# Kernel tuning notes

Measured on AMD Instinct MI355X. Metric: run time of the kernel, lower is better.

The kernel has to match this reference:

```python
import jax, jax.numpy as jnp
import numpy as np
from jax import lax

B, N, W = 32, 512, 256
C = 16            # branch channels; D = 4*C = 64
Z = 8             # SAE latent
E = 8             # sensor embedding dim
HD = 16           # GAT head dim = max(8, 32//2)
GOUT = 32         # GAT out dim
TOPK = 20
RHO, EPS = 0.05, 1e-6
KS = [2, 3, 5, 7]


def _glorot(key, shape):
    fan_in, fan_out = shape[0], shape[-1]
    lim = jnp.sqrt(6.0 / (fan_in + fan_out))
    return jax.random.uniform(key, shape, jnp.float32, -lim, lim)


def setup_inputs() -> dict:
    key = jax.random.key(0)
    ks = jax.random.split(key, 32)
    inp = {"x": jax.random.normal(ks[0], (B, N, W), jnp.float32)}
    # MSTCN conv weights: torch Conv1d weight [C, 1, k], bias [C]
    for i, k in enumerate(KS):
        inp[f"conv_w{k}"] = jax.random.normal(ks[1 + i], (C, 1, k), jnp.float32) * (1.0 / np.sqrt(k))
        inp[f"conv_b{k}"] = jnp.zeros((C,), jnp.float32)
    inp["enc_w"] = _glorot(ks[6], (4 * C, Z));  inp["enc_b"] = jnp.zeros((Z,), jnp.float32)
    inp["dec_w"] = _glorot(ks[7], (Z, W));      inp["dec_b"] = jnp.zeros((W,), jnp.float32)
    inp["sensor_emb"] = _glorot(ks[8], (N, E))
    gin = Z + E
    inp["gat0_w"] = _glorot(ks[9], (gin, HD))
    inp["gat0_asrc"] = _glorot(ks[10], (1, HD))[0]
    inp["gat0_adst"] = _glorot(ks[11], (1, HD))[0]
    inp["gat1_w"] = _glorot(ks[12], (gin, HD))
    inp["gat1_asrc"] = _glorot(ks[13], (1, HD))[0]
    inp["gat1_adst"] = _glorot(ks[14], (1, HD))[0]
    inp["proj_w"] = _glorot(ks[15], (2 * HD, GOUT)); inp["proj_b"] = jnp.zeros((GOUT,), jnp.float32)
    inp["head_w"] = _glorot(ks[16], (GOUT, 1));      inp["head_b"] = jnp.zeros((1,), jnp.float32)
    return inp


def _mstcn(x, convs):
    # x: [B,N,W] -> node_feat [B,N,4C]
    b, n, w = x.shape
    xr = x.reshape(b * n, 1, w)
    feats = []
    for (cw, cb), k in zip(convs, KS):
        pl = (k - 1) // 2
        pr = (k - 1) - pl
        y = lax.conv_general_dilated(xr, cw, (1,), [(pl, pr)],
                                     dimension_numbers=("NCH", "OIH", "NCH"))
        y = y + cb[None, :, None]                 # [B*N, C, W]
        feats.append(y.mean(-1).reshape(b, n, C)) # time mean -> [B,N,C]
    return jnp.concatenate(feats, -1)


def _graph_learning(sensor_emb):
    # returns A [N,N]
    nrm = jnp.sqrt(jnp.sum(sensor_emb * sensor_emb, -1, keepdims=True))
    emb = sensor_emb / jnp.maximum(nrm, 1e-12)
    sim = (emb @ emb.T) / jnp.sqrt(jnp.float32(E))
    n = sim.shape[0]
    sim_ns = sim.at[jnp.diag_indices(n)].set(-jnp.inf)
    idx = lax.top_k(sim_ns, TOPK)[1]                       # [N, topk]
    mask = jnp.zeros_like(sim).at[jnp.arange(n)[:, None], idx].set(1.0)
    return jax.nn.relu(sim) * mask + jnp.eye(n, dtype=sim.dtype)


def _gat_head(x, a, w, a_src, a_dst):
    # x [B,N,F], a [N,N] -> [B,N,HD]; eval mode (dropout off)
    h = x @ w                                   # [B,N,HD]
    e_src = h @ a_src                           # [B,N]
    e_dst = h @ a_dst                           # [B,N]
    e = jax.nn.leaky_relu(e_src[:, :, None] + e_dst[:, None, :], 0.2)  # [B,N,N]
    e = jnp.where((a > 0)[None], e, -jnp.inf)
    alpha = jax.nn.softmax(e, axis=-1)
    return alpha @ h


def reference(x, conv_w2, conv_b2, conv_w3, conv_b3, conv_w5, conv_b5,
              conv_w7, conv_b7, enc_w, enc_b, dec_w, dec_b, sensor_emb,
              gat0_w, gat0_asrc, gat0_adst, gat1_w, gat1_asrc, gat1_adst,
              proj_w, proj_b, head_w, head_b):
    convs = [(conv_w2, conv_b2), (conv_w3, conv_b3), (conv_w5, conv_b5), (conv_w7, conv_b7)]
    node_feat = _mstcn(x, convs)                           # [B,N,64]
    # Sparse autoencoder
    z = node_feat @ enc_w + enc_b                          # [B,N,Z]
    recon = z @ dec_w + dec_b                              # [B,N,W]
    act = jax.nn.sigmoid(z)
    rho_hat = jnp.clip(act.mean((0, 1)), EPS, 1.0 - EPS)
    kl = jnp.sum(RHO * jnp.log(RHO / rho_hat) + (1.0 - RHO) * jnp.log((1.0 - RHO) / (1.0 - rho_hat)))
    sparsity_dev = jnp.mean(jnp.abs(act - RHO), -1)        # [B,N]
    # Graph learning + GAT
    a = _graph_learning(sensor_emb)                        # [N,N]
    e_b = jnp.broadcast_to(sensor_emb[None], (x.shape[0], N, E))
    gat_in = jnp.concatenate([z, e_b], -1)                 # [B,N,Z+E]
    h0 = _gat_head(gat_in, a, gat0_w, gat0_asrc, gat0_adst)
    h1 = _gat_head(gat_in, a, gat1_w, gat1_asrc, gat1_adst)
    h = jnp.concatenate([h0, h1], -1)
    fused = jax.nn.elu(h @ proj_w + proj_b)                # [B,N,GOUT]
    predicted = (fused @ head_w + head_b)[..., 0]          # [B,N]
    return predicted, recon, kl, sparsity_dev
```

## Files before the change

### kernel.cpp

```cpp
#include <hip/hip_runtime.h>
#include <math.h>

#define B_   32
#define N_   512
#define W_   256
#define BN_  (B_*N_)
#define NBLK_A 2048
#define RHOG   2048

__device__ __forceinline__ float wave_reduce_sum64(float v) {
#pragma unroll
    for (int m = 32; m >= 1; m >>= 1) v += __shfl_xor(v, m);
    return v;
}

__global__ __launch_bounds__(256) void kPre(
    const float* __restrict__ se,
    const float* __restrict__ w2, const float* __restrict__ b2,
    const float* __restrict__ w3, const float* __restrict__ b3,
    const float* __restrict__ w5, const float* __restrict__ b5,
    const float* __restrict__ w7, const float* __restrict__ b7,
    const float* __restrict__ enc_w, const float* __restrict__ enc_b,
    const float* __restrict__ g0w, const float* __restrict__ g0s, const float* __restrict__ g0d,
    const float* __restrict__ g1w, const float* __restrict__ g1s, const float* __restrict__ g1d,
    float* __restrict__ en_g, float* __restrict__ ws_gam,
    float* __restrict__ ws_gsz, float* __restrict__ ws_gA)
{
    const int tid = threadIdx.x;

    if (blockIdx.x == 0) {
#pragma unroll
        for (int p = 0; p < 2; ++p) {
            const int rr = tid + p * 256;
            const float4 a = reinterpret_cast<const float4*>(se)[rr * 2];
            const float4 b = reinterpret_cast<const float4*>(se)[rr * 2 + 1];
            const float ss = a.x*a.x + a.y*a.y + a.z*a.z + a.w*a.w
                           + b.x*b.x + b.y*b.y + b.z*b.z + b.w*b.w;
            const float inv = 1.0f / fmaxf(sqrtf(ss), 1e-12f);
            float4 oa = a, ob = b;
            oa.x*=inv; oa.y*=inv; oa.z*=inv; oa.w*=inv;
            ob.x*=inv; ob.y*=inv; ob.z*=inv; ob.w*=inv;
            reinterpret_cast<float4*>(en_g)[rr * 2]     = oa;
            reinterpret_cast<float4*>(en_g)[rr * 2 + 1] = ob;
        }
        return;
    }

    __shared__ float L[1432];
    const int oW2=0, oW3=32, oW5=80, oW7=160;
    const int oB2=272, oB3=288, oB5=304, oB7=320;
    const int oEW=336, oEB=848, oG0=856, oG1=1112, oAV=1368;
#define CPY(off, src, n) for (int t = tid; t < (n); t += 256) L[(off)+t] = (src)[t];
    CPY(oW2, w2, 32)  CPY(oW3, w3, 48)  CPY(oW5, w5, 80)  CPY(oW7, w7, 112)
    CPY(oB2, b2, 16)  CPY(oB3, b3, 16)  CPY(oB5, b5, 16)  CPY(oB7, b7, 16)
    CPY(oEW, enc_w, 512)  CPY(oEB, enc_b, 8)
    CPY(oG0, g0w, 256)    CPY(oG1, g1w, 256)
    CPY(oAV, g0s, 16) CPY(oAV+16, g0d, 16) CPY(oAV+32, g1s, 16) CPY(oAV+48, g1d, 16)
#undef CPY
    __syncthreads();

    if (tid < 64) {
        const int zi = tid & 7, t = tid >> 3;
        float acc = (t == 7) ? L[oEB + zi] : 0.f;
#define GAM_KI(BASE_C, OFFW, OFFB, KK)                                          \
        {                                                                       \
            const int k = KK; const int pl = (k - 1) >> 1;                      \
            _Pragma("unroll")                                                   \
            for (int ch = 0; ch < 16; ++ch) {                                   \
                float a;                                                        \
                if (t == 7) a = L[OFFB + ch];                                   \
                else if (t == 0) {                                              \
                    a = 0.f;                                                    \
                    _Pragma("unroll")                                           \
                    for (int j = 0; j < k; ++j) a += L[OFFW + ch*k + j];        \
                    a *= (1.f/(float)W_);                                       \
                } else if (t <= 3) {                                            \
                    const int j = pl + t;                                       \
                    a = (j < k) ? -L[OFFW + ch*k + j]*(1.f/(float)W_) : 0.f;    \
                } else {                                                        \
                    const int j = pl - (t - 3);                                 \
                    a = (j >= 0) ? -L[OFFW + ch*k + j]*(1.f/(float)W_) : 0.f;   \
                }                                                               \
                acc += a * L[oEW + (BASE_C + ch)*8 + zi];                       \
            }                                                                   \
        }
        GAM_KI(0,  oW2, oB2, 2)
        GAM_KI(16, oW3, oB3, 3)
        GAM_KI(32, oW5, oB5, 5)
        GAM_KI(48, oW7, oB7, 7)
#undef GAM_KI
        ws_gam[zi*8+t] = acc;
    } else if (tid < 96) {
        const int q = (tid-64) >> 3, f = (tid-64) & 7;
        const int gw = (q >> 1) ? oG1 : oG0;
        const int av = oAV + q*16;
        float v = 0.f;
#pragma unroll
        for (int d = 0; d < 16; ++d) v += L[gw + f*16+d] * L[av + d];
        ws_gsz[q*8+f] = v;
    } else if (tid < 128) {
        const int q = (tid-96) >> 3, f = (tid-96) & 7;
        const int gw = (q >> 1) ? oG1 : oG0;
        const int av = oAV + q*16;
        float v = 0.f;
#pragma unroll
        for (int d = 0; d < 16; ++d) v += L[gw + (8+f)*16+d] * L[av + d];
        ws_gA[q*8+f] = v;
    }
}

__global__ __launch_bounds__(256) void kTop(const float* __restrict__ en_g,
                                            int* __restrict__ adj)
{
    const int wave = threadIdx.x >> 6;
    const int lane = threadIdx.x & 63;
    const int i = (blockIdx.x << 2) + wave;

    const float4 ei0 = reinterpret_cast<const float4*>(en_g)[i * 2];
    const float4 ei1 = reinterpret_cast<const float4*>(en_g)[i * 2 + 1];

    float v[8];
#pragma unroll
    for (int q = 0; q < 8; ++q) {
        const int j = (q << 6) + lane;
        const float4 a = reinterpret_cast<const float4*>(en_g)[j * 2];
        const float4 b = reinterpret_cast<const float4*>(en_g)[j * 2 + 1];
        const float d = ei0.x*a.x + ei0.y*a.y + ei0.z*a.z + ei0.w*a.w
                      + ei1.x*b.x + ei1.y*b.y + ei1.z*b.z + ei1.w*b.w;
        v[q] = (j == i) ? -3.4e38f : d * 0.35355339059327373f;
    }

    int cnt = 1;
    if (lane == 0) adj[i * 24 + 1] = i;
    for (int it = 0; it < 20; ++it) {
        float bv = v[0]; int bq = 0;
#pragma unroll
        for (int q = 1; q < 8; ++q) if (v[q] > bv) { bv = v[q]; bq = q; }
        int bj = (bq << 6) + lane;
#pragma unroll
        for (int m = 32; m >= 1; m >>= 1) {
            const float ov = __shfl_xor(bv, m);
            const int   oj = __shfl_xor(bj, m);
            if (ov > bv || (ov == bv && oj < bj)) { bv = ov; bj = oj; }
        }
        if (bv <= 0.f) break;
        if (lane == 0) adj[i * 24 + 1 + cnt] = bj;
        cnt++;
        const int wq = bj >> 6, wl = bj & 63;
#pragma unroll
        for (int q = 0; q < 8; ++q) if (q == wq && lane == wl) v[q] = -3.4e38f;
    }
    if (lane == 0) adj[i * 24] = cnt;
}

__global__ __launch_bounds__(256) void kA(
    const float* __restrict__ x,
    const float* __restrict__ dec_w, const float* __restrict__ dec_b,
    const float* __restrict__ g0w, const float* __restrict__ g1w,
    const float* __restrict__ se,
    const float* __restrict__ ws_gam, const float* __restrict__ ws_gsz,
    const float* __restrict__ ws_gA,
    float* __restrict__ out_recon, float* __restrict__ out_sdev,
    float* __restrict__ ws_h, float* __restrict__ ws_e, float* __restrict__ ws_rho)
{
    __shared__ float lds_rho[4][8];
    const int wave = threadIdx.x >> 6;
    const int lane = threadIdx.x & 63;
    const int r0 = (blockIdx.x << 3) + (wave << 1);
    const int n0 = r0 & (N_ - 1), n1 = (r0 + 1) & (N_ - 1);

    const float4 xv0 = reinterpret_cast<const float4*>(x)[(size_t)r0 * 64 + lane];
    const float4 xv1 = reinterpret_cast<const float4*>(x)[(size_t)(r0+1) * 64 + lane];
    const float4 ph0 = reinterpret_cast<const float4*>(x)[(size_t)r0 * 64];
    const float4 pt0 = reinterpret_cast<const float4*>(x)[(size_t)r0 * 64 + 63];
    const float4 ph1 = reinterpret_cast<const float4*>(x)[(size_t)(r0+1) * 64];
    const float4 pt1 = reinterpret_cast<const float4*>(x)[(size_t)(r0+1) * 64 + 63];

    float S0 = xv0.x + xv0.y + xv0.z + xv0.w;
    float S1 = xv1.x + xv1.y + xv1.z + xv1.w;
#pragma unroll
    for (int m = 32; m >= 1; m >>= 1) { S0 += __shfl_xor(S0, m); S1 += __shfl_xor(S1, m); }

    const float P10 = ph0.x, P20 = P10 + ph0.y, P30 = P20 + ph0.z;
    const float Q10 = pt0.w, Q20 = Q10 + pt0.z, Q30 = Q20 + pt0.y;
    const float P11 = ph1.x, P21 = P11 + ph1.y, P31 = P21 + ph1.z;
    const float Q11 = pt1.w, Q21 = Q11 + pt1.z, Q31 = Q21 + pt1.y;

    float z0[8], z1[8];
#pragma unroll
    for (int zi = 0; zi < 8; ++zi) {
        const float4 g0 = reinterpret_cast<const float4*>(ws_gam)[zi * 2];
        const float4 g1 = reinterpret_cast<const float4*>(ws_gam)[zi * 2 + 1];
        z0[zi] = g1.w + g0.x*S0 + g0.y*P10 + g0.z*P20 + g0.w*P30
                       + g1.x*Q10 + g1.y*Q20 + g1.z*Q30;
        z1[zi] = g1.w + g0.x*S1 + g0.y*P11 + g0.z*P21 + g0.w*P31
                       + g1.x*Q11 + g1.y*Q21 + g1.z*Q31;
    }

    {
        const float4 db = reinterpret_cast<const float4*>(dec_b)[lane];
        float4 rec0 = db, rec1 = db;
#pragma unroll
        for (int zi = 0; zi < 8; ++zi) {
            const float4 dw = reinterpret_cast<const float4*>(dec_w)[zi * 64 + lane];
            rec0.x += z0[zi]*dw.x; rec0.y += z0[zi]*dw.y; rec0.z += z0[zi]*dw.z; rec0.w += z0[zi]*dw.w;
            rec1.x += z1[zi]*dw.x; rec1.y += z1[zi]*dw.y; rec1.z += z1[zi]*dw.z; rec1.w += z1[zi]*dw.w;
        }
        reinterpret_cast<float4*>(out_recon)[(size_t)r0 * 64 + lane] = rec0;
        reinterpret_cast<float4*>(out_recon)[(size_t)(r0+1) * 64 + lane] = rec1;
    }

    if (lane < 16) {
        const int zi = lane & 7;
        const int rr = lane >> 3;
        float zl = 0.f;
#pragma unroll
        for (int p = 0; p < 8; ++p)
            zl = (zi == p) ? (rr ? z1[p] : z0[p]) : zl;
        const float a = 1.0f / (1.0f + __expf(-zl));
        float sd = fabsf(a - 0.05f);
        sd += __shfl_xor(sd, 1); sd += __shfl_xor(sd, 2); sd += __shfl_xor(sd, 4);
        if (zi == 0) out_sdev[r0 + rr] = sd * 0.125f;
        const float rho = a + __shfl_xor(a, 8);
        if (lane < 8) lds_rho[wave][lane] = rho;
    }

    if (lane < 32) {
        const float* gw = (lane >> 4) ? g1w : g0w;
        const int dd = lane & 15;
        float gwz[16];
#pragma unroll
        for (int f = 0; f < 16; ++f) gwz[f] = gw[f * 16 + dd];
        float h0 = 0.f, h1 = 0.f;
#pragma unroll
        for (int f = 0; f < 8; ++f) { h0 += z0[f] * gwz[f]; h1 += z1[f] * gwz[f]; }
#pragma unroll
        for (int f = 0; f < 8; ++f) {
            h0 += se[n0 * 8 + f] * gwz[8 + f];
            h1 += se[n1 * 8 + f] * gwz[8 + f];
        }
        ws_h[(size_t)r0 * 32 + lane] = h0;
        ws_h[(size_t)(r0+1) * 32 + lane] = h1;
    } else if (lane < 40) {
        const int q = (lane - 32) & 3;
        const int rr = (lane - 32) >> 2;
        const int nn = rr ? n1 : n0;
        float v = 0.f;
#pragma unroll
        for (int f = 0; f < 8; ++f) v += se[nn * 8 + f] * ws_gA[q * 8 + f];
#pragma unroll
        for (int f = 0; f < 8; ++f) v += (rr ? z1[f] : z0[f]) * ws_gsz[q * 8 + f];
        ws_e[(size_t)(r0 + rr) * 4 + q] = v;
    }

    __syncthreads();
    if (threadIdx.x < 8) {
        const float t = lds_rho[0][threadIdx.x] + lds_rho[1][threadIdx.x]
                      + lds_rho[2][threadIdx.x] + lds_rho[3][threadIdx.x];
        ws_rho[(size_t)blockIdx.x * 8 + threadIdx.x] = t;
    }
}

__global__ __launch_bounds__(256) void kD(
    const float* __restrict__ ws_h, const float* __restrict__ ws_e,
    const int* __restrict__ adj,
    const float* __restrict__ proj_w, const float* __restrict__ proj_b,
    const float* __restrict__ head_w, const float* __restrict__ head_b,
    float* __restrict__ out_pred,
    const float* __restrict__ ws_rho, float* __restrict__ out_kl)
{
    __shared__ float red[4][8];
    const int lane = threadIdx.x & 63;
    const int wave = threadIdx.x >> 6;
    const int half = lane >> 5;
    const int t32 = lane & 31;
    const int ri = (wave << 1) + half;
    const int r = (blockIdx.x << 3) + ri;
    const int b = r >> 9;
    const int i = r & (N_ - 1);
    const int cnt = adj[i * 24];

    const float4 er = reinterpret_cast<const float4*>(ws_e)[r];

    const int j = (t32 < cnt) ? adj[i * 24 + 1 + t32] : i;
    const int rj = (b << 9) | j;
    const float4 ejv = reinterpret_cast<const float4*>(ws_e)[rj];
    float e0 = er.x + ejv.y;  e0 = (e0 >= 0.f) ? e0 : 0.2f * e0;
    float e1 = er.z + ejv.w;  e1 = (e1 >= 0.f) ? e1 : 0.2f * e1;
    if (t32 >= cnt) { e0 = -3.4e38f; e1 = -3.4e38f; }
    float m0 = e0, m1 = e1;
#pragma unroll
    for (int m = 16; m >= 1; m >>= 1) {
        m0 = fmaxf(m0, __shfl_xor(m0, m));
        m1 = fmaxf(m1, __shfl_xor(m1, m));
    }
    float w0 = (t32 < cnt) ? __expf(e0 - m0) : 0.f;
    float w1 = (t32 < cnt) ? __expf(e1 - m1) : 0.f;
    float s0 = w0, s1 = w1;
#pragma unroll
    for (int m = 16; m >= 1; m >>= 1) {
        s0 += __shfl_xor(s0, m);
        s1 += __shfl_xor(s1, m);
    }

    const int d = t32;
    const int head = d >> 4;
    const float sinv = 1.0f / (head ? s1 : s0);
    float acc = 0.f;
#pragma unroll
    for (int t = 0; t < 21; ++t) {
        const float wt0 = __shfl(w0, t, 32);
        const float wt1 = __shfl(w1, t, 32);
        const int   jt  = __shfl(j, t, 32);
        const float wt  = head ? wt1 : wt0;
        acc += wt * ws_h[(size_t)((b << 9) | jt) * 32 + d];
    }
    const float hval = acc * sinv;

    float f = proj_b[d];
#pragma unroll
    for (int dd = 0; dd < 32; ++dd) {
        const float hv = __shfl(hval, dd, 32);
        f += hv * proj_w[dd * 32 + d];
    }
    f = (f > 0.f) ? f : expm1f(f);
    float p = f * head_w[d];
#pragma unroll
    for (int mm = 16; mm >= 1; mm >>= 1) p += __shfl_xor(p, mm);
    if (d == 0) out_pred[r] = p + head_b[0];

    if (blockIdx.x == 0) {
        float t8[8] = {0, 0, 0, 0, 0, 0, 0, 0};
        for (int g = (int)threadIdx.x; g < RHOG; g += 256) {
            const float4 a  = reinterpret_cast<const float4*>(ws_rho)[g * 2];
            const float4 bb = reinterpret_cast<const float4*>(ws_rho)[g * 2 + 1];
            t8[0] += a.x;  t8[1] += a.y;  t8[2] += a.z;  t8[3] += a.w;
            t8[4] += bb.x; t8[5] += bb.y; t8[6] += bb.z; t8[7] += bb.w;
        }
#pragma unroll
        for (int m = 32; m >= 1; m >>= 1)
#pragma unroll
            for (int zi = 0; zi < 8; ++zi) t8[zi] += __shfl_xor(t8[zi], m);
        if (lane == 0) {
#pragma unroll
            for (int zi = 0; zi < 8; ++zi) red[wave][zi] = t8[zi];
        }
        __syncthreads();
        if (threadIdx.x == 0) {
            float kl = 0.f;
#pragma unroll
            for (int zi = 0; zi < 8; ++zi) {
                float rh = (red[0][zi] + red[1][zi] + red[2][zi] + red[3][zi])
                           * (1.0f / (float)BN_);
                rh = fminf(fmaxf(rh, 1e-6f), 1.0f - 1e-6f);
                kl += 0.05f * logf(0.05f / rh) + 0.95f * logf(0.95f / (1.0f - rh));
            }
            out_kl[0] = kl;
        }
    }
}

extern "C" void kernel_launch(void* const* d_in, const int* in_sizes, int n_in,
                              void* d_out, int out_size, void* d_ws, size_t ws_size,
                              hipStream_t stream)
{
    (void)in_sizes; (void)n_in; (void)out_size; (void)ws_size;
    const float* x     = (const float*)d_in[0];
    const float* w2    = (const float*)d_in[1];
    const float* b2    = (const float*)d_in[2];
    const float* w3    = (const float*)d_in[3];
    const float* b3    = (const float*)d_in[4];
    const float* w5    = (const float*)d_in[5];
    const float* b5    = (const float*)d_in[6];
    const float* w7    = (const float*)d_in[7];
    const float* b7    = (const float*)d_in[8];
    const float* enc_w = (const float*)d_in[9];
    const float* enc_b = (const float*)d_in[10];
    const float* dec_w = (const float*)d_in[11];
    const float* dec_b = (const float*)d_in[12];
    const float* se    = (const float*)d_in[13];
    const float* g0w   = (const float*)d_in[14];
    const float* g0s   = (const float*)d_in[15];
    const float* g0d   = (const float*)d_in[16];
    const float* g1w   = (const float*)d_in[17];
    const float* g1s   = (const float*)d_in[18];
    const float* g1d   = (const float*)d_in[19];
    const float* pw    = (const float*)d_in[20];
    const float* pb    = (const float*)d_in[21];
    const float* hw    = (const float*)d_in[22];
    const float* hb    = (const float*)d_in[23];

    float* out       = (float*)d_out;
    float* out_pred  = out;
    float* out_recon = out + 16384;
    float* out_kl    = out + 16384 + 4194304;
    float* out_sdev  = out_kl + 1;

    float* ws_h   = (float*)d_ws;
    float* ws_e   = ws_h   + (size_t)BN_ * 32;
    float* ws_rho = ws_e   + (size_t)BN_ * 4;
    float* ws_gam = ws_rho + (size_t)RHOG * 8;
    float* ws_gsz = ws_gam + 64;
    float* ws_gA  = ws_gsz + 32;
    float* ws_en  = ws_gA  + 32;
    int*   ws_adj = (int*)(ws_en + (size_t)N_ * 8);

    hipLaunchKernelGGL(kPre, dim3(2), dim3(256), 0, stream,
                       se, w2, b2, w3, b3, w5, b5, w7, b7, enc_w, enc_b,
                       g0w, g0s, g0d, g1w, g1s, g1d,
                       ws_en, ws_gam, ws_gsz, ws_gA);
    hipLaunchKernelGGL(kTop, dim3(N_ / 4), dim3(256), 0, stream, ws_en, ws_adj);
    hipLaunchKernelGGL(kA, dim3(NBLK_A), dim3(256), 0, stream,
                       x, dec_w, dec_b, g0w, g1w, se,
                       ws_gam, ws_gsz, ws_gA,
                       out_recon, out_sdev, ws_h, ws_e, ws_rho);
    hipLaunchKernelGGL(kD, dim3(BN_ / 8), dim3(256), 0, stream,
                       ws_h, ws_e, ws_adj, pw, pb, hw, hb, out_pred,
                       ws_rho, out_kl);
}
```

Measured before the change: 58.87 us.

## Fuse preprocessing, top-k graph build and main encoder into one kernel launch

Merges kPre, kTop and kA into a single kernel. Extra blocks run the top-k neighbour search and normalise the embeddings inline. Every encoder block recomputes the small folded weight tables (gam, gsz, gA) into shared memory instead of reading them from a global workspace. This removes two kernel launches and their serialising dependencies, letting the top-k work overlap with the main pass. In exchange, each of the 2048 blocks repeats the weight-table setup and adds a block barrier, and the top-k blocks redo the norm computation for every candidate.

```diff
diff --git a/kernel.cpp b/kernel.cpp
--- a/kernel.cpp
+++ b/kernel.cpp
@@ -6,47 +6,79 @@
 #define W_   256
 #define BN_  (B_*N_)
 #define NBLK_A 2048
+#define NBLK_T 128
 #define RHOG   2048
 
-__device__ __forceinline__ float wave_reduce_sum64(float v) {
-#pragma unroll
-    for (int m = 32; m >= 1; m >>= 1) v += __shfl_xor(v, m);
-    return v;
-}
-
-__global__ __launch_bounds__(256) void kPre(
-    const float* __restrict__ se,
+__global__ __launch_bounds__(256) void kMain(
+    const float* __restrict__ x,
     const float* __restrict__ w2, const float* __restrict__ b2,
     const float* __restrict__ w3, const float* __restrict__ b3,
     const float* __restrict__ w5, const float* __restrict__ b5,
     const float* __restrict__ w7, const float* __restrict__ b7,
     const float* __restrict__ enc_w, const float* __restrict__ enc_b,
+    const float* __restrict__ dec_w, const float* __restrict__ dec_b,
+    const float* __restrict__ se,
     const float* __restrict__ g0w, const float* __restrict__ g0s, const float* __restrict__ g0d,
     const float* __restrict__ g1w, const float* __restrict__ g1s, const float* __restrict__ g1d,
-    float* __restrict__ en_g, float* __restrict__ ws_gam,
-    float* __restrict__ ws_gsz, float* __restrict__ ws_gA)
+    float* __restrict__ out_recon, float* __restrict__ out_sdev,
+    float* __restrict__ ws_h, float* __restrict__ ws_e, float* __restrict__ ws_rho,
+    int* __restrict__ adj)
 {
-    const int tid = threadIdx.x;
-
-    if (blockIdx.x == 0) {
-#pragma unroll
-        for (int p = 0; p < 2; ++p) {
-            const int rr = tid + p * 256;
-            const float4 a = reinterpret_cast<const float4*>(se)[rr * 2];
-            const float4 b = reinterpret_cast<const float4*>(se)[rr * 2 + 1];
-            const float ss = a.x*a.x + a.y*a.y + a.z*a.z + a.w*a.w
-                           + b.x*b.x + b.y*b.y + b.z*b.z + b.w*b.w;
-            const float inv = 1.0f / fmaxf(sqrtf(ss), 1e-12f);
-            float4 oa = a, ob = b;
-            oa.x*=inv; oa.y*=inv; oa.z*=inv; oa.w*=inv;
-            ob.x*=inv; ob.y*=inv; ob.z*=inv; ob.w*=inv;
-            reinterpret_cast<float4*>(en_g)[rr * 2]     = oa;
-            reinterpret_cast<float4*>(en_g)[rr * 2 + 1] = ob;
-        }
+    const int tid  = threadIdx.x;
+    const int wave = tid >> 6;
+    const int lane = tid & 63;
+
+    if (blockIdx.x >= NBLK_A) {
+        const int i = ((blockIdx.x - NBLK_A) << 2) + wave;
+        const float4 a_i = reinterpret_cast<const float4*>(se)[i * 2];
+        const float4 b_i = reinterpret_cast<const float4*>(se)[i * 2 + 1];
+        const float ssi = a_i.x*a_i.x + a_i.y*a_i.y + a_i.z*a_i.z + a_i.w*a_i.w
+                        + b_i.x*b_i.x + b_i.y*b_i.y + b_i.z*b_i.z + b_i.w*b_i.w;
+        const float inv_i = 1.0f / fmaxf(sqrtf(ssi), 1e-12f);
+
+        float v[8];
+#pragma unroll
+        for (int q = 0; q < 8; ++q) {
+            const int j = (q << 6) + lane;
+            const float4 a = reinterpret_cast<const float4*>(se)[j * 2];
+            const float4 b = reinterpret_cast<const float4*>(se)[j * 2 + 1];
+            const float d = a_i.x*a.x + a_i.y*a.y + a_i.z*a.z + a_i.w*a.w
+                          + b_i.x*b.x + b_i.y*b.y + b_i.z*b.z + b_i.w*b.w;
+            const float ssj = a.x*a.x + a.y*a.y + a.z*a.z + a.w*a.w
+                            + b.x*b.x + b.y*b.y + b.z*b.z + b.w*b.w;
+            const float inv_j = 1.0f / fmaxf(sqrtf(ssj), 1e-12f);
+            v[q] = (j == i) ? -3.4e38f
+                            : d * inv_i * inv_j * 0.35355339059327373f;
+        }
+        int cnt = 1;
+        if (lane == 0) adj[i * 24 + 1] = i;
+        for (int it = 0; it < 20; ++it) {
+            float bv = v[0]; int bq = 0;
+#pragma unroll
+            for (int q = 1; q < 8; ++q) if (v[q] > bv) { bv = v[q]; bq = q; }
+            int bj = (bq << 6) + lane;
+#pragma unroll
+            for (int m = 32; m >= 1; m >>= 1) {
+                const float ov = __shfl_xor(bv, m);
+                const int   oj = __shfl_xor(bj, m);
+                if (ov > bv || (ov == bv && oj < bj)) { bv = ov; bj = oj; }
+            }
+            if (bv <= 0.f) break;
+            if (lane == 0) adj[i * 24 + 1 + cnt] = bj;
+            cnt++;
+            const int wq = bj >> 6, wl = bj & 63;
+#pragma unroll
+            for (int q = 0; q < 8; ++q) if (q == wq && lane == wl) v[q] = -3.4e38f;
+        }
+        if (lane == 0) adj[i * 24] = cnt;
         return;
     }
 
     __shared__ float L[1432];
+    __shared__ __align__(16) float sGam[64];
+    __shared__ float sGsz[32];
+    __shared__ float sGA[32];
+    __shared__ float lds_rho[4][8];
     const int oW2=0, oW3=32, oW5=80, oW7=160;
     const int oB2=272, oB3=288, oB5=304, oB7=320;
     const int oEW=336, oEB=848, oG0=856, oG1=1112, oAV=1368;
@@ -89,7 +121,7 @@
         GAM_KI(32, oW5, oB5, 5)
         GAM_KI(48, oW7, oB7, 7)
 #undef GAM_KI
-        ws_gam[zi*8+t] = acc;
+        sGam[zi*8+t] = acc;
     } else if (tid < 96) {
         const int q = (tid-64) >> 3, f = (tid-64) & 7;
         const int gw = (q >> 1) ? oG1 : oG0;
@@ -97,7 +129,7 @@
         float v = 0.f;
 #pragma unroll
         for (int d = 0; d < 16; ++d) v += L[gw + f*16+d] * L[av + d];
-        ws_gsz[q*8+f] = v;
+        sGsz[q*8+f] = v;
     } else if (tid < 128) {
         const int q = (tid-96) >> 3, f = (tid-96) & 7;
         const int gw = (q >> 1) ? oG1 : oG0;
@@ -105,67 +137,10 @@
         float v = 0.f;
 #pragma unroll
         for (int d = 0; d < 16; ++d) v += L[gw + (8+f)*16+d] * L[av + d];
-        ws_gA[q*8+f] = v;
-    }
-}
-
-__global__ __launch_bounds__(256) void kTop(const float* __restrict__ en_g,
-                                            int* __restrict__ adj)
-{
-    const int wave = threadIdx.x >> 6;
-    const int lane = threadIdx.x & 63;
-    const int i = (blockIdx.x << 2) + wave;
-
-    const float4 ei0 = reinterpret_cast<const float4*>(en_g)[i * 2];
-    const float4 ei1 = reinterpret_cast<const float4*>(en_g)[i * 2 + 1];
-
-    float v[8];
-#pragma unroll
-    for (int q = 0; q < 8; ++q) {
-        const int j = (q << 6) + lane;
-        const float4 a = reinterpret_cast<const float4*>(en_g)[j * 2];
-        const float4 b = reinterpret_cast<const float4*>(en_g)[j * 2 + 1];
-        const float d = ei0.x*a.x + ei0.y*a.y + ei0.z*a.z + ei0.w*a.w
-                      + ei1.x*b.x + ei1.y*b.y + ei1.z*b.z + ei1.w*b.w;
-        v[q] = (j == i) ? -3.4e38f : d * 0.35355339059327373f;
-    }
-
-    int cnt = 1;
-    if (lane == 0) adj[i * 24 + 1] = i;
-    for (int it = 0; it < 20; ++it) {
-        float bv = v[0]; int bq = 0;
-#pragma unroll
-        for (int q = 1; q < 8; ++q) if (v[q] > bv) { bv = v[q]; bq = q; }
-        int bj = (bq << 6) + lane;
-#pragma unroll
-        for (int m = 32; m >= 1; m >>= 1) {
-            const float ov = __shfl_xor(bv, m);
-            const int   oj = __shfl_xor(bj, m);
-            if (ov > bv || (ov == bv && oj < bj)) { bv = ov; bj = oj; }
-        }
-        if (bv <= 0.f) break;
-        if (lane == 0) adj[i * 24 + 1 + cnt] = bj;
-        cnt++;
-        const int wq = bj >> 6, wl = bj & 63;
-#pragma unroll
-        for (int q = 0; q < 8; ++q) if (q == wq && lane == wl) v[q] = -3.4e38f;
-    }
-    if (lane == 0) adj[i * 24] = cnt;
-}
-
-__global__ __launch_bounds__(256) void kA(
-    const float* __restrict__ x,
-    const float* __restrict__ dec_w, const float* __restrict__ dec_b,
-    const float* __restrict__ g0w, const float* __restrict__ g1w,
-    const float* __restrict__ se,
-    const float* __restrict__ ws_gam, const float* __restrict__ ws_gsz,
-    const float* __restrict__ ws_gA,
-    float* __restrict__ out_recon, float* __restrict__ out_sdev,
-    float* __restrict__ ws_h, float* __restrict__ ws_e, float* __restrict__ ws_rho)
-{
-    __shared__ float lds_rho[4][8];
-    const int wave = threadIdx.x >> 6;
-    const int lane = threadIdx.x & 63;
+        sGA[q*8+f] = v;
+    }
+    __syncthreads();
+
     const int r0 = (blockIdx.x << 3) + (wave << 1);
     const int n0 = r0 & (N_ - 1), n1 = (r0 + 1) & (N_ - 1);
 
@@ -189,8 +164,8 @@
     float z0[8], z1[8];
 #pragma unroll
     for (int zi = 0; zi < 8; ++zi) {
-        const float4 g0 = reinterpret_cast<const float4*>(ws_gam)[zi * 2];
-        const float4 g1 = reinterpret_cast<const float4*>(ws_gam)[zi * 2 + 1];
+        const float4 g0 = reinterpret_cast<const float4*>(sGam)[zi * 2];
+        const float4 g1 = reinterpret_cast<const float4*>(sGam)[zi * 2 + 1];
         z0[zi] = g1.w + g0.x*S0 + g0.y*P10 + g0.z*P20 + g0.w*P30
                        + g1.x*Q10 + g1.y*Q20 + g1.z*Q30;
         z1[zi] = g1.w + g0.x*S1 + g0.y*P11 + g0.z*P21 + g0.w*P31
@@ -226,11 +201,11 @@
     }
 
     if (lane < 32) {
-        const float* gw = (lane >> 4) ? g1w : g0w;
+        const int gw = (lane >> 4) ? oG1 : oG0;
         const int dd = lane & 15;
         float gwz[16];
 #pragma unroll
-        for (int f = 0; f < 16; ++f) gwz[f] = gw[f * 16 + dd];
+        for (int f = 0; f < 16; ++f) gwz[f] = L[gw + f * 16 + dd];
         float h0 = 0.f, h1 = 0.f;
 #pragma unroll
         for (int f = 0; f < 8; ++f) { h0 += z0[f] * gwz[f]; h1 += z1[f] * gwz[f]; }
@@ -247,17 +222,17 @@
         const int nn = rr ? n1 : n0;
         float v = 0.f;
 #pragma unroll
-        for (int f = 0; f < 8; ++f) v += se[nn * 8 + f] * ws_gA[q * 8 + f];
-#pragma unroll
-        for (int f = 0; f < 8; ++f) v += (rr ? z1[f] : z0[f]) * ws_gsz[q * 8 + f];
+        for (int f = 0; f < 8; ++f) v += se[nn * 8 + f] * sGA[q * 8 + f];
+#pragma unroll
+        for (int f = 0; f < 8; ++f) v += (rr ? z1[f] : z0[f]) * sGsz[q * 8 + f];
         ws_e[(size_t)(r0 + rr) * 4 + q] = v;
     }
 
     __syncthreads();
-    if (threadIdx.x < 8) {
-        const float t = lds_rho[0][threadIdx.x] + lds_rho[1][threadIdx.x]
-                      + lds_rho[2][threadIdx.x] + lds_rho[3][threadIdx.x];
-        ws_rho[(size_t)blockIdx.x * 8 + threadIdx.x] = t;
+    if (tid < 8) {
+        const float t = lds_rho[0][tid] + lds_rho[1][tid]
+                      + lds_rho[2][tid] + lds_rho[3][tid];
+        ws_rho[(size_t)blockIdx.x * 8 + tid] = t;
     }
 }
 
@@ -399,21 +374,12 @@
     float* ws_h   = (float*)d_ws;
     float* ws_e   = ws_h   + (size_t)BN_ * 32;
     float* ws_rho = ws_e   + (size_t)BN_ * 4;
-    float* ws_gam = ws_rho + (size_t)RHOG * 8;
-    float* ws_gsz = ws_gam + 64;
-    float* ws_gA  = ws_gsz + 32;
-    float* ws_en  = ws_gA  + 32;
-    int*   ws_adj = (int*)(ws_en + (size_t)N_ * 8);
-
-    hipLaunchKernelGGL(kPre, dim3(2), dim3(256), 0, stream,
-                       se, w2, b2, w3, b3, w5, b5, w7, b7, enc_w, enc_b,
-                       g0w, g0s, g0d, g1w, g1s, g1d,
-                       ws_en, ws_gam, ws_gsz, ws_gA);
-    hipLaunchKernelGGL(kTop, dim3(N_ / 4), dim3(256), 0, stream, ws_en, ws_adj);
-    hipLaunchKernelGGL(kA, dim3(NBLK_A), dim3(256), 0, stream,
-                       x, dec_w, dec_b, g0w, g1w, se,
-                       ws_gam, ws_gsz, ws_gA,
-                       out_recon, out_sdev, ws_h, ws_e, ws_rho);
+    int*   ws_adj = (int*)(ws_rho + (size_t)RHOG * 8);
+
+    hipLaunchKernelGGL(kMain, dim3(NBLK_A + NBLK_T), dim3(256), 0, stream,
+                       x, w2, b2, w3, b3, w5, b5, w7, b7, enc_w, enc_b,
+                       dec_w, dec_b, se, g0w, g0s, g0d, g1w, g1s, g1d,
+                       out_recon, out_sdev, ws_h, ws_e, ws_rho, ws_adj);
     hipLaunchKernelGGL(kD, dim3(BN_ / 8), dim3(256), 0, stream,
                        ws_h, ws_e, ws_adj, pw, pb, hw, hb, out_pred,
                        ws_rho, out_kl);
```

New measurement: 66.14 us. +12.4%, slower.
